# Kernel optimization log

Measured on AMD Instinct MI355X. Metric: run time of the kernel, lower is better.

The kernel has to match this reference:

```python
import jax, jax.numpy as jnp
import numpy as np

INPUT_DIM = 64
HIDDEN = 256
BATCH = 256
SEQ = 512
LN_EPS = 1e-5


def setup_inputs() -> dict:
    key = jax.random.key(0)
    ks = jax.random.split(key, 10)
    def lin(k, fan_in, fan_out):
        bound = 1.0 / np.sqrt(fan_in)
        kw, kb = jax.random.split(k)
        W = jax.random.uniform(kw, (fan_in, fan_out), jnp.float32, -bound, bound)
        b = jax.random.uniform(kb, (fan_out,), jnp.float32, -bound, bound)
        return W, b
    x = jax.random.normal(ks[0], (BATCH, SEQ, INPUT_DIM), jnp.float32)
    # layer 0: input_dim -> hidden
    Wz0, bz0 = lin(ks[1], INPUT_DIM + HIDDEN, 3 * HIDDEN)
    Wc0, bc0 = lin(ks[2], INPUT_DIM + HIDDEN, HIDDEN)
    # layer 1: hidden -> hidden
    Wz1, bz1 = lin(ks[3], HIDDEN + HIDDEN, 3 * HIDDEN)
    Wc1, bc1 = lin(ks[4], HIDDEN + HIDDEN, HIDDEN)
    ln_gamma = jnp.ones((HIDDEN,), jnp.float32)
    ln_beta = jnp.zeros((HIDDEN,), jnp.float32)
    return {"x": x, "Wz0": Wz0, "bz0": bz0, "Wc0": Wc0, "bc0": bc0,
            "Wz1": Wz1, "bz1": bz1, "Wc1": Wc1, "bc1": bc1,
            "ln_gamma": ln_gamma, "ln_beta": ln_beta}


def _gru_cell(h, x_t, Wz, bz, Wc, bc):
    # combined = [h, x]  (hidden first, as in the torch code)
    combined = jnp.concatenate([h, x_t], axis=-1)
    gates = combined @ Wz + bz  # (B, 3H); third chunk is unused (as in source)
    z = jax.nn.sigmoid(gates[:, :HIDDEN])
    r = jax.nn.sigmoid(gates[:, HIDDEN:2 * HIDDEN])
    reset_combined = jnp.concatenate([r * h, x_t], axis=-1)
    h_tilde = jnp.tanh(reset_combined @ Wc + bc)
    return (1.0 - z) * h + z * h_tilde


def reference(x, Wz0, bz0, Wc0, bc0, Wz1, bz1, Wc1, bc1, ln_gamma, ln_beta):
    # sanitize: NaN -> 0, Inf -> sign * 10
    x = jnp.where(jnp.isnan(x), 0.0, x)
    x = jnp.where(jnp.isinf(x), jnp.sign(x) * 10.0, x)

    B = x.shape[0]
    h0 = jnp.zeros((B, HIDDEN), x.dtype)
    h1 = jnp.zeros((B, HIDDEN), x.dtype)

    def step(carry, x_t):
        h0, h1 = carry
        h0 = _gru_cell(h0, x_t, Wz0, bz0, Wc0, bc0)
        h1 = _gru_cell(h1, h0, Wz1, bz1, Wc1, bc1)
        return (h0, h1), None

    xs = jnp.swapaxes(x, 0, 1)  # (seq, batch, input_dim)
    (h0, h1), _ = jax.lax.scan(step, (h0, h1), xs)

    # LayerNorm on final top-layer hidden state
    mean = jnp.mean(h1, axis=-1, keepdims=True)
    var = jnp.var(h1, axis=-1, keepdims=True)
    enc = (h1 - mean) * jax.lax.rsqrt(var + LN_EPS) * ln_gamma + ln_beta
    return enc
```

## Files before the change

kernel.cpp:

```cpp
#include <hip/hip_runtime.h>


#define SEQL 512
#define CH 8
#define NCH 64
#define DEPTH 4

#define RB0  1310720u
#define GSTR 1048576u
#define CTRB (RB0 + 16u * GSTR)

typedef __bf16 bf16x8 __attribute__((ext_vector_type(8)));
typedef float f32x4 __attribute__((ext_vector_type(4)));
typedef unsigned int u32x4 __attribute__((ext_vector_type(4)));
typedef unsigned long long u64;

__device__ __forceinline__ unsigned short f2bf(float f) {
  unsigned int u = __builtin_bit_cast(unsigned int, f);
  u += 0x7fffu + ((u >> 16) & 1u);
  return (unsigned short)(u >> 16);
}
__device__ __forceinline__ float bf2f(unsigned short u) {
  unsigned int v = ((unsigned int)u) << 16;
  return __builtin_bit_cast(float, v);
}
__device__ __forceinline__ float sigm(float x) { return 1.0f / (1.0f + __expf(-x)); }
__device__ __forceinline__ float tanh_(float x) { return 1.0f - 2.0f / (__expf(2.0f * x) + 1.0f); }
__device__ __forceinline__ float sanit(float v) {
  if (!(v == v)) return 0.f;
  if (isinf(v)) return v > 0.f ? 10.f : -10.f;
  return v;
}

__device__ __forceinline__ void st8(u64* p, u64 v) {
  __hip_atomic_store(p, v, __ATOMIC_RELAXED, __HIP_MEMORY_SCOPE_AGENT);
}

__device__ __forceinline__ void ld_frame8(const unsigned short* base, int lane, u32x4* c) {
  const char* p0 = (const char*)base + lane * 16;
  const char* p4 = p0 + 4096;
  asm volatile(
      "global_load_dwordx4 %0, %8, off sc0 sc1\n\t"
      "global_load_dwordx4 %1, %8, off offset:1024 sc0 sc1\n\t"
      "global_load_dwordx4 %2, %8, off offset:2048 sc0 sc1\n\t"
      "global_load_dwordx4 %3, %8, off offset:3072 sc0 sc1\n\t"
      "global_load_dwordx4 %4, %9, off sc0 sc1\n\t"
      "global_load_dwordx4 %5, %9, off offset:1024 sc0 sc1\n\t"
      "global_load_dwordx4 %6, %9, off offset:2048 sc0 sc1\n\t"
      "global_load_dwordx4 %7, %9, off offset:3072 sc0 sc1\n\t"
      "s_waitcnt vmcnt(0)"
      : "=&v"(c[0]), "=&v"(c[1]), "=&v"(c[2]), "=&v"(c[3]),
        "=&v"(c[4]), "=&v"(c[5]), "=&v"(c[6]), "=&v"(c[7])
      : "v"(p0), "v"(p4)
      : "memory");
}
__device__ __forceinline__ void ld_part12(const unsigned short* pf, int wave, int lane,
                                          u64* z, u64* r, u64* c) {
  const char* p0 = (const char*)pf + ((4 * wave) * 64 + lane) * 8;
  const char* p1 = p0 + 8192;
  const char* p2 = p0 + 16384;
  asm volatile(
      "global_load_dwordx2 %0, %12, off sc0 sc1\n\t"
      "global_load_dwordx2 %1, %12, off offset:512 sc0 sc1\n\t"
      "global_load_dwordx2 %2, %12, off offset:1024 sc0 sc1\n\t"
      "global_load_dwordx2 %3, %12, off offset:1536 sc0 sc1\n\t"
      "global_load_dwordx2 %4, %13, off sc0 sc1\n\t"
      "global_load_dwordx2 %5, %13, off offset:512 sc0 sc1\n\t"
      "global_load_dwordx2 %6, %13, off offset:1024 sc0 sc1\n\t"
      "global_load_dwordx2 %7, %13, off offset:1536 sc0 sc1\n\t"
      "global_load_dwordx2 %8, %14, off sc0 sc1\n\t"
      "global_load_dwordx2 %9, %14, off offset:512 sc0 sc1\n\t"
      "global_load_dwordx2 %10, %14, off offset:1024 sc0 sc1\n\t"
      "global_load_dwordx2 %11, %14, off offset:1536 sc0 sc1\n\t"
      "s_waitcnt vmcnt(0)"
      : "=&v"(z[0]), "=&v"(z[1]), "=&v"(z[2]), "=&v"(z[3]),
        "=&v"(r[0]), "=&v"(r[1]), "=&v"(r[2]), "=&v"(r[3]),
        "=&v"(c[0]), "=&v"(c[1]), "=&v"(c[2]), "=&v"(c[3])
      : "v"(p0), "v"(p1), "v"(p2)
      : "memory");
}

__global__ __launch_bounds__(256) void prep_weights(
    const float* __restrict__ Wz0, const float* __restrict__ Wc0,
    const float* __restrict__ Wz1, const float* __restrict__ Wc1,
    unsigned short* __restrict__ ws) {
  int idx = blockIdx.x * 256 + threadIdx.x;
  const float* W;
  int stride, KT, base;
  if (idx < 163840)      { W = Wz0; stride = 768; KT = 10; base = 0; }
  else if (idx < 245760) { W = Wc0; stride = 256; KT = 10; base = 163840; idx -= 163840; }
  else if (idx < 507904) { W = Wz1; stride = 768; KT = 16; base = 245760; idx -= 245760; }
  else                   { W = Wc1; stride = 256; KT = 16; base = 507904; idx -= 507904; }
  int tile = idx >> 9;
  int t = idx & 511;
  int nt = tile / KT;
  int kt = tile - nt * KT;
  int n15 = t & 15;
  int klocal = t >> 4;
  int k = (kt << 5) + klocal;
  int n = (nt << 4) + n15;
  int lane = ((klocal >> 3) << 4) | n15;
  int j = klocal & 7;
  ws[base + (tile << 9) + (lane << 3) + j] = f2bf(W[k * stride + n]);
}

__device__ __forceinline__ void waitge(int* p, int v, int tid) {
  __syncthreads();
  if (tid == 0) {
    long it = 0;
    while (__hip_atomic_load(p, __ATOMIC_RELAXED, __HIP_MEMORY_SCOPE_AGENT) < v) {
      __builtin_amdgcn_s_sleep(1);
      if (++it > (1L << 24)) break;
    }
  }
  __syncthreads();
}
__device__ __forceinline__ void publish(int* p, int v, int tid) {
  asm volatile("s_waitcnt vmcnt(0)" ::: "memory");
  __syncthreads();
  if (tid == 0) __hip_atomic_store(p, v, __ATOMIC_RELAXED, __HIP_MEMORY_SCOPE_AGENT);
}

#define DLOC(c) ((((c) >> 5) << 9) + (((((c) >> 3) & 3) << 4) + (quad << 2)) * 8 + ((c) & 7))
#define MFMA(a, b, c) __builtin_amdgcn_mfma_f32_16x16x32_bf16((a), (b), (c), 0, 0, 0)

union UB  { u32x4 q; bf16x8 v; };
union UB8 { u64 q; ushort4 s; };

__global__ __launch_bounds__(256, 1) void gru_pipe(
    const float* __restrict__ x,
    const float* __restrict__ bz0, const float* __restrict__ bc0,
    const float* __restrict__ bz1, const float* __restrict__ bc1,
    const float* __restrict__ gamma, const float* __restrict__ beta,
    const unsigned short* __restrict__ wsw,
    unsigned short* __restrict__ gws,
    float* __restrict__ out) {
  __shared__ __align__(16) unsigned short lds[75776];
  const int tid  = threadIdx.x;
  const int wave = tid >> 6;
  const int lane = tid & 63;
  const int l15  = lane & 15;
  const int quad = lane >> 4;
  const int stage = blockIdx.x >> 4;
  const int g     = blockIdx.x & 15;
  const int row0  = g << 4;

  const bf16x8* __restrict__ wsv = (const bf16x8*)wsw;
  unsigned short* ringh = gws + (RB0 >> 1) + (size_t)g * (GSTR >> 1);
  unsigned short* ringp = ringh + 131072;
  int* ctr = (int*)((char*)gws + CTRB) + g * 16;

  if (stage == 0) {
    unsigned short* h0f  = lds;
    unsigned short* rh0f = lds + 4096;
    unsigned short* xf   = lds + 8192;
    unsigned short* xw   = lds + 10240;
    unsigned short* cw0  = lds + 59392;
    for (int u = tid; u < 6144; u += 256) {
      int flat = u << 3, ti = flat >> 9, q = flat & 511, srct;
      if (ti < 64) srct = (ti >> 1) * 10 + 8 + (ti & 1);
      else         srct = 320 + ((ti - 64) >> 1) * 10 + 8 + (ti & 1);
      *(uint4*)(xw + flat) = *(const uint4*)(wsw + srct * 512 + q);
    }
    for (int u = tid; u < 2048; u += 256) {
      int flat = u << 3, ti = flat >> 9, q = flat & 511;
      int srct = 320 + (ti >> 1) * 10 + 6 + (ti & 1);
      *(uint4*)(cw0 + flat) = *(const uint4*)(wsw + srct * 512 + q);
    }
    for (int i = tid; i < 4096; i += 256) h0f[i] = 0;

    bf16x8 pz[4][8], pr[4][8], pc[4][6];
#pragma unroll
    for (int j = 0; j < 4; ++j) {
      const int zt = 4 * wave + j;
#pragma unroll
      for (int k = 0; k < 8; ++k) {
        pz[j][k] = wsv[(zt * 10 + k) * 64 + lane];
        pr[j][k] = wsv[((16 + zt) * 10 + k) * 64 + lane];
      }
#pragma unroll
      for (int k = 0; k < 6; ++k)
        pc[j][k] = wsv[(320 + zt * 10 + k) * 64 + lane];
    }
#pragma unroll
    for (int j = 0; j < 4; ++j) {
#pragma unroll
      for (int k = 0; k < 8; ++k)
        asm volatile("" : "+a"(pz[j][k]), "+a"(pr[j][k]));
#pragma unroll
      for (int k = 0; k < 6; ++k)
        asm volatile("" : "+v"(pc[j][k]));
    }

    float bzz[4], bzr[4], bcc[4];
    int dloc[4];
#pragma unroll
    for (int j = 0; j < 4; ++j) {
      const int col = 64 * wave + 16 * j + l15;
      bzz[j] = bz0[col]; bzr[j] = bz0[256 + col]; bcc[j] = bc0[col];
      dloc[j] = DLOC(col);
    }
    f32x4 h0s[4] = {{0,0,0,0},{0,0,0,0},{0,0,0,0},{0,0,0,0}};

    const int xrow = tid >> 4, c4 = (tid & 15) << 2;
    const float* xp = x + (size_t)(row0 + xrow) * (SEQL * 64) + c4;
    const int xbase = ((c4 >> 5) << 9) + ((((c4 >> 3) & 3) << 4) + xrow) * 8 + (c4 & 7);
    {
      float4 xv = *(const float4*)xp;
      xf[xbase] = f2bf(sanit(xv.x)); xf[xbase + 1] = f2bf(sanit(xv.y));
      xf[xbase + 2] = f2bf(sanit(xv.z)); xf[xbase + 3] = f2bf(sanit(xv.w));
    }
    __syncthreads();

    for (int ch = 0; ch < NCH; ++ch) {
      if (ch >= DEPTH) waitge(ctr + 2, ch - (DEPTH - 1), tid);
      unsigned short* slot = ringh + (ch & (DEPTH - 1)) * (CH * 4096);
      for (int s = 0; s < CH; ++s) {
        const int t = (ch << 3) + s;
        if (s > 0) {
          u64* dst = (u64*)(slot + (s - 1) * 4096);
          const u64* src = (const u64*)h0f;
#pragma unroll
          for (int q = 0; q < 4; ++q) st8(dst + tid + 256 * q, src[tid + 256 * q]);
        }
        const unsigned short* xb = xf + ((t & 1) << 10);
        const bool havex = (t + 1 < SEQL);
        float4 xn;
        if (havex) xn = *(const float4*)(xp + (t + 1) * 64);

        f32x4 za[4], ra[4];
#pragma unroll
        for (int j = 0; j < 4; ++j) { za[j] = {bzz[j],bzz[j],bzz[j],bzz[j]}; ra[j] = {bzr[j],bzr[j],bzr[j],bzr[j]}; }
#pragma unroll
        for (int k = 0; k < 8; ++k) {
          bf16x8 a = *(const bf16x8*)(h0f + (k << 9) + (lane << 3));
#pragma unroll
          for (int j = 0; j < 4; ++j) { za[j] = MFMA(a, pz[j][k], za[j]); ra[j] = MFMA(a, pr[j][k], ra[j]); }
        }
#pragma unroll
        for (int k = 0; k < 2; ++k) {
          bf16x8 a = *(const bf16x8*)(xb + (k << 9) + (lane << 3));
#pragma unroll
          for (int j = 0; j < 4; ++j) {
            bf16x8 bz_ = *(const bf16x8*)(xw + ((((4 * wave + j) << 1) | k) << 9) + (lane << 3));
            bf16x8 br_ = *(const bf16x8*)(xw + ((((16 + 4 * wave + j) << 1) | k) << 9) + (lane << 3));
            za[j] = MFMA(a, bz_, za[j]); ra[j] = MFMA(a, br_, ra[j]);
          }
        }
        float zg[4][4];
#pragma unroll
        for (int j = 0; j < 4; ++j)
#pragma unroll
          for (int i = 0; i < 4; ++i) {
            zg[j][i] = sigm(za[j][i]);
            rh0f[dloc[j] + i * 8] = f2bf(sigm(ra[j][i]) * h0s[j][i]);
          }
        __syncthreads();

        f32x4 ca[4];
#pragma unroll
        for (int j = 0; j < 4; ++j) ca[j] = {bcc[j],bcc[j],bcc[j],bcc[j]};
#pragma unroll
        for (int k = 0; k < 6; ++k) {
          bf16x8 a = *(const bf16x8*)(rh0f + (k << 9) + (lane << 3));
#pragma unroll
          for (int j = 0; j < 4; ++j) ca[j] = MFMA(a, pc[j][k], ca[j]);
        }
#pragma unroll
        for (int kk = 0; kk < 2; ++kk) {
          bf16x8 a = *(const bf16x8*)(rh0f + ((6 + kk) << 9) + (lane << 3));
#pragma unroll
          for (int j = 0; j < 4; ++j) {
            bf16x8 bc_ = *(const bf16x8*)(cw0 + ((((4 * wave + j) << 1) | kk) << 9) + (lane << 3));
            ca[j] = MFMA(a, bc_, ca[j]);
          }
        }
#pragma unroll
        for (int k = 0; k < 2; ++k) {
          bf16x8 a = *(const bf16x8*)(xb + (k << 9) + (lane << 3));
#pragma unroll
          for (int j = 0; j < 4; ++j) {
            bf16x8 bc_ = *(const bf16x8*)(xw + 32768 + ((((4 * wave + j) << 1) | k) << 9) + (lane << 3));
            ca[j] = MFMA(a, bc_, ca[j]);
          }
        }
#pragma unroll
        for (int j = 0; j < 4; ++j)
#pragma unroll
          for (int i = 0; i < 4; ++i) {
            float ht = tanh_(ca[j][i]);
            float hn = h0s[j][i] + zg[j][i] * (ht - h0s[j][i]);
            h0s[j][i] = hn;
            h0f[dloc[j] + i * 8] = f2bf(hn);
          }
        if (havex) {
          unsigned short* xb1 = xf + (((t + 1) & 1) << 10);
          xb1[xbase] = f2bf(sanit(xn.x)); xb1[xbase + 1] = f2bf(sanit(xn.y));
          xb1[xbase + 2] = f2bf(sanit(xn.z)); xb1[xbase + 3] = f2bf(sanit(xn.w));
        }
        __syncthreads();
      }
      {
        u64* dst = (u64*)(slot + 7 * 4096);
        const u64* src = (const u64*)h0f;
#pragma unroll
        for (int q = 0; q < 4; ++q) st8(dst + tid + 256 * q, src[tid + 256 * q]);
      }
      publish(ctr + 0, ch + 1, tid);
    }
  } else if (stage == 1) {
    unsigned short* cwB = lds;
    for (int u = tid; u < 2048; u += 256) {
      int flat = u << 3, ti = flat >> 9, q = flat & 511;
      int srct = 992 + (ti >> 1) * 16 + 14 + (ti & 1);
      *(uint4*)(cwB + flat) = *(const uint4*)(wsw + srct * 512 + q);
    }
    __syncthreads();

    bf16x8 p1[4][8], p2[4][8], p3[4][6];
#pragma unroll
    for (int j = 0; j < 4; ++j) {
      const int nt = 4 * wave + j;
#pragma unroll
      for (int k = 0; k < 8; ++k) {
        p1[j][k] = wsv[(480 + nt * 16 + 8 + k) * 64 + lane];
        p2[j][k] = wsv[(480 + (16 + nt) * 16 + 8 + k) * 64 + lane];
      }
#pragma unroll
      for (int k = 0; k < 6; ++k)
        p3[j][k] = wsv[(992 + nt * 16 + 8 + k) * 64 + lane];
    }
#pragma unroll
    for (int j = 0; j < 4; ++j) {
#pragma unroll
      for (int k = 0; k < 8; ++k)
        asm volatile("" : "+a"(p1[j][k]), "+a"(p2[j][k]));
#pragma unroll
      for (int k = 0; k < 6; ++k)
        asm volatile("" : "+v"(p3[j][k]));
    }
    float b1[4], b2[4], b3[4];
#pragma unroll
    for (int j = 0; j < 4; ++j) {
      const int col = 64 * wave + 16 * j + l15;
      b1[j] = bz1[col]; b2[j] = bz1[256 + col]; b3[j] = bc1[col];
    }
    for (int ch = 0; ch < NCH; ++ch) {
      waitge(ctr + 0, ch + 1, tid);
      if (ch >= DEPTH) waitge(ctr + 3, ch - (DEPTH - 1), tid);
      const unsigned short* hslot = ringh + (ch & (DEPTH - 1)) * (CH * 4096);
      unsigned short* pslot = ringp + (ch & (DEPTH - 1)) * (CH * 12288);
      for (int s = 0; s < CH; ++s) {
        u32x4 cf[8];
        ld_frame8(hslot + s * 4096, lane, cf);
        f32x4 za[4] = {{0,0,0,0},{0,0,0,0},{0,0,0,0},{0,0,0,0}};
        f32x4 ra[4] = {{0,0,0,0},{0,0,0,0},{0,0,0,0},{0,0,0,0}};
        f32x4 ca[4] = {{0,0,0,0},{0,0,0,0},{0,0,0,0},{0,0,0,0}};
#pragma unroll
        for (int k = 0; k < 8; ++k) {
          UB ub; ub.q = cf[k];
          bf16x8 a = ub.v;
#pragma unroll
          for (int j = 0; j < 4; ++j) {
            za[j] = MFMA(a, p1[j][k], za[j]);
            ra[j] = MFMA(a, p2[j][k], ra[j]);
            if (k < 6) ca[j] = MFMA(a, p3[j][k], ca[j]);
          }
        }
#pragma unroll
        for (int kk = 0; kk < 2; ++kk) {
          UB ub; ub.q = cf[6 + kk];
          bf16x8 a = ub.v;
#pragma unroll
          for (int j = 0; j < 4; ++j) {
            bf16x8 bc_ = *(const bf16x8*)(cwB + ((((4 * wave + j) << 1) | kk) << 9) + (lane << 3));
            ca[j] = MFMA(a, bc_, ca[j]);
          }
        }
        u64* pf = (u64*)(pslot + s * 12288);
#pragma unroll
        for (int j = 0; j < 4; ++j) {
          ushort4 vz, vr, vc;
          vz.x = f2bf(za[j][0] + b1[j]); vz.y = f2bf(za[j][1] + b1[j]);
          vz.z = f2bf(za[j][2] + b1[j]); vz.w = f2bf(za[j][3] + b1[j]);
          vr.x = f2bf(ra[j][0] + b2[j]); vr.y = f2bf(ra[j][1] + b2[j]);
          vr.z = f2bf(ra[j][2] + b2[j]); vr.w = f2bf(ra[j][3] + b2[j]);
          vc.x = f2bf(ca[j][0] + b3[j]); vc.y = f2bf(ca[j][1] + b3[j]);
          vc.z = f2bf(ca[j][2] + b3[j]); vc.w = f2bf(ca[j][3] + b3[j]);
          st8(pf + (4 * wave + j) * 64 + lane,      __builtin_bit_cast(u64, vz));
          st8(pf + (16 + 4 * wave + j) * 64 + lane, __builtin_bit_cast(u64, vr));
          st8(pf + (32 + 4 * wave + j) * 64 + lane, __builtin_bit_cast(u64, vc));
        }
      }
      publish(ctr + 1, ch + 1, tid);
      if (tid == 0)
        __hip_atomic_store(ctr + 2, ch + 1, __ATOMIC_RELAXED, __HIP_MEMORY_SCOPE_AGENT);
    }
  } else {
    unsigned short* h1f  = lds;
    unsigned short* rh1f = lds + 4096;
    unsigned short* cwC  = lds + 8192;
    for (int u = tid; u < 2048; u += 256) {
      int flat = u << 3, ti = flat >> 9, q = flat & 511;
      int srct = 992 + (ti >> 1) * 16 + 6 + (ti & 1);
      *(uint4*)(cwC + flat) = *(const uint4*)(wsw + srct * 512 + q);
    }
    bf16x8 q1[4][8], q2[4][8], q3[4][6];
#pragma unroll
    for (int j = 0; j < 4; ++j) {
      const int nt = 4 * wave + j;
#pragma unroll
      for (int k = 0; k < 8; ++k) {
        q1[j][k] = wsv[(480 + nt * 16 + k) * 64 + lane];
        q2[j][k] = wsv[(480 + (16 + nt) * 16 + k) * 64 + lane];
      }
#pragma unroll
      for (int k = 0; k < 6; ++k)
        q3[j][k] = wsv[(992 + nt * 16 + k) * 64 + lane];
    }
#pragma unroll
    for (int j = 0; j < 4; ++j) {
#pragma unroll
      for (int k = 0; k < 8; ++k)
        asm volatile("" : "+a"(q1[j][k]), "+a"(q2[j][k]));
#pragma unroll
      for (int k = 0; k < 6; ++k)
        asm volatile("" : "+v"(q3[j][k]));
    }
    for (int i = tid; i < 4096; i += 256) h1f[i] = 0;
    int dloc[4];
#pragma unroll
    for (int j = 0; j < 4; ++j) dloc[j] = DLOC(64 * wave + 16 * j + l15);
    f32x4 h1s[4] = {{0,0,0,0},{0,0,0,0},{0,0,0,0},{0,0,0,0}};
    __syncthreads();

    for (int ch = 0; ch < NCH; ++ch) {
      waitge(ctr + 1, ch + 1, tid);
      const unsigned short* pslot = ringp + (ch & (DEPTH - 1)) * (CH * 12288);
      for (int s = 0; s < CH; ++s) {
        u64 zq[4], rq[4], cq[4];
        ld_part12(pslot + s * 12288, wave, lane, zq, rq, cq);
        f32x4 za[4] = {{0,0,0,0},{0,0,0,0},{0,0,0,0},{0,0,0,0}};
        f32x4 ra[4] = {{0,0,0,0},{0,0,0,0},{0,0,0,0},{0,0,0,0}};
#pragma unroll
        for (int k = 0; k < 8; ++k) {
          bf16x8 a = *(const bf16x8*)(h1f + (k << 9) + (lane << 3));
#pragma unroll
          for (int j = 0; j < 4; ++j) { za[j] = MFMA(a, q1[j][k], za[j]); ra[j] = MFMA(a, q2[j][k], ra[j]); }
        }
        float zg[4][4];
#pragma unroll
        for (int j = 0; j < 4; ++j) {
          UB8 uz, ur; uz.q = zq[j]; ur.q = rq[j];
#pragma unroll
          for (int i = 0; i < 4; ++i) {
            zg[j][i] = sigm(za[j][i] + bf2f(((const unsigned short*)&uz.s)[i]));
            float r = sigm(ra[j][i] + bf2f(((const unsigned short*)&ur.s)[i]));
            rh1f[dloc[j] + i * 8] = f2bf(r * h1s[j][i]);
          }
        }
        __syncthreads();

        f32x4 ca[4] = {{0,0,0,0},{0,0,0,0},{0,0,0,0},{0,0,0,0}};
#pragma unroll
        for (int k = 0; k < 6; ++k) {
          bf16x8 a = *(const bf16x8*)(rh1f + (k << 9) + (lane << 3));
#pragma unroll
          for (int j = 0; j < 4; ++j) ca[j] = MFMA(a, q3[j][k], ca[j]);
        }
#pragma unroll
        for (int kk = 0; kk < 2; ++kk) {
          bf16x8 a = *(const bf16x8*)(rh1f + ((6 + kk) << 9) + (lane << 3));
#pragma unroll
          for (int j = 0; j < 4; ++j) {
            bf16x8 bc_ = *(const bf16x8*)(cwC + ((((4 * wave + j) << 1) | kk) << 9) + (lane << 3));
            ca[j] = MFMA(a, bc_, ca[j]);
          }
        }
#pragma unroll
        for (int j = 0; j < 4; ++j) {
          UB8 uc; uc.q = cq[j];
#pragma unroll
          for (int i = 0; i < 4; ++i) {
            float ht = tanh_(ca[j][i] + bf2f(((const unsigned short*)&uc.s)[i]));
            float hn = h1s[j][i] + zg[j][i] * (ht - h1s[j][i]);
            h1s[j][i] = hn;
            h1f[dloc[j] + i * 8] = f2bf(hn);
          }
        }
        __syncthreads();
      }
      publish(ctr + 3, ch + 1, tid);
    }

    float* h1buf = (float*)lds;
#pragma unroll
    for (int j = 0; j < 4; ++j)
#pragma unroll
      for (int i = 0; i < 4; ++i)
        h1buf[(quad * 4 + i) * 256 + 64 * wave + 16 * j + l15] = h1s[j][i];
    __syncthreads();

    const int r = tid >> 4, cl = tid & 15;
    float v[16], s = 0.f, sq = 0.f;
#pragma unroll
    for (int jj = 0; jj < 16; ++jj) {
      v[jj] = h1buf[r * 256 + cl + (jj << 4)];
      s += v[jj]; sq += v[jj] * v[jj];
    }
#pragma unroll
    for (int off = 8; off > 0; off >>= 1) {
      s  += __shfl_xor(s, off);
      sq += __shfl_xor(sq, off);
    }
    const float mean = s * (1.f / 256.f);
    const float var  = sq * (1.f / 256.f) - mean * mean;
    const float rstd = rsqrtf(var + 1e-5f);
    float* op = out + (size_t)(row0 + r) * 256;
#pragma unroll
    for (int jj = 0; jj < 16; ++jj) {
      const int c = cl + (jj << 4);
      op[c] = (v[jj] - mean) * rstd * gamma[c] + beta[c];
    }
  }
}

extern "C" void kernel_launch(void* const* d_in, const int* in_sizes, int n_in,
                              void* d_out, int out_size, void* d_ws, size_t ws_size,
                              hipStream_t stream) {
  const float* x     = (const float*)d_in[0];
  const float* Wz0   = (const float*)d_in[1];
  const float* bz0   = (const float*)d_in[2];
  const float* Wc0   = (const float*)d_in[3];
  const float* bc0   = (const float*)d_in[4];
  const float* Wz1   = (const float*)d_in[5];
  const float* bz1   = (const float*)d_in[6];
  const float* Wc1   = (const float*)d_in[7];
  const float* bc1   = (const float*)d_in[8];
  const float* gamma = (const float*)d_in[9];
  const float* beta  = (const float*)d_in[10];
  unsigned short* ws = (unsigned short*)d_ws;
  float* out = (float*)d_out;

  hipMemsetAsync((char*)d_ws + CTRB, 0, 1024, stream);
  hipLaunchKernelGGL(prep_weights, dim3(2496), dim3(256), 0, stream, Wz0, Wc0, Wz1, Wc1, ws);
  hipLaunchKernelGGL(gru_pipe, dim3(48), dim3(256), 0, stream,
                     x, bz0, bc0, bz1, bc1, gamma, beta, ws, ws, out);
}
```

Measured before the change: 2.629 ms.

## Double workgroup size to 8 waves, halving output column tiles per wave

Result: faster. 2.331 ms (-11.3%).

```diff
diff --git a/kernel.cpp b/kernel.cpp
--- a/kernel.cpp
+++ b/kernel.cpp
@@ -54,28 +54,21 @@
       : "v"(p0), "v"(p4)
       : "memory");
 }
-__device__ __forceinline__ void ld_part12(const unsigned short* pf, int wave, int lane,
-                                          u64* z, u64* r, u64* c) {
-  const char* p0 = (const char*)pf + ((4 * wave) * 64 + lane) * 8;
+__device__ __forceinline__ void ld_part6(const unsigned short* pf, int wave, int lane,
+                                         u64* z, u64* r, u64* c) {
+  const char* p0 = (const char*)pf + ((2 * wave) * 64 + lane) * 8;
   const char* p1 = p0 + 8192;
   const char* p2 = p0 + 16384;
   asm volatile(
-      "global_load_dwordx2 %0, %12, off sc0 sc1\n\t"
-      "global_load_dwordx2 %1, %12, off offset:512 sc0 sc1\n\t"
-      "global_load_dwordx2 %2, %12, off offset:1024 sc0 sc1\n\t"
-      "global_load_dwordx2 %3, %12, off offset:1536 sc0 sc1\n\t"
-      "global_load_dwordx2 %4, %13, off sc0 sc1\n\t"
-      "global_load_dwordx2 %5, %13, off offset:512 sc0 sc1\n\t"
-      "global_load_dwordx2 %6, %13, off offset:1024 sc0 sc1\n\t"
-      "global_load_dwordx2 %7, %13, off offset:1536 sc0 sc1\n\t"
-      "global_load_dwordx2 %8, %14, off sc0 sc1\n\t"
-      "global_load_dwordx2 %9, %14, off offset:512 sc0 sc1\n\t"
-      "global_load_dwordx2 %10, %14, off offset:1024 sc0 sc1\n\t"
-      "global_load_dwordx2 %11, %14, off offset:1536 sc0 sc1\n\t"
+      "global_load_dwordx2 %0, %6, off sc0 sc1\n\t"
+      "global_load_dwordx2 %1, %6, off offset:512 sc0 sc1\n\t"
+      "global_load_dwordx2 %2, %7, off sc0 sc1\n\t"
+      "global_load_dwordx2 %3, %7, off offset:512 sc0 sc1\n\t"
+      "global_load_dwordx2 %4, %8, off sc0 sc1\n\t"
+      "global_load_dwordx2 %5, %8, off offset:512 sc0 sc1\n\t"
       "s_waitcnt vmcnt(0)"
-      : "=&v"(z[0]), "=&v"(z[1]), "=&v"(z[2]), "=&v"(z[3]),
-        "=&v"(r[0]), "=&v"(r[1]), "=&v"(r[2]), "=&v"(r[3]),
-        "=&v"(c[0]), "=&v"(c[1]), "=&v"(c[2]), "=&v"(c[3])
+      : "=&v"(z[0]), "=&v"(z[1]), "=&v"(r[0]), "=&v"(r[1]),
+        "=&v"(c[0]), "=&v"(c[1])
       : "v"(p0), "v"(p1), "v"(p2)
       : "memory");
 }
@@ -127,7 +120,7 @@
 union UB  { u32x4 q; bf16x8 v; };
 union UB8 { u64 q; ushort4 s; };
 
-__global__ __launch_bounds__(256, 1) void gru_pipe(
+__global__ __launch_bounds__(512, 2) void gru_pipe(
     const float* __restrict__ x,
     const float* __restrict__ bz0, const float* __restrict__ bc0,
     const float* __restrict__ bz1, const float* __restrict__ bc1,
@@ -156,23 +149,23 @@
     unsigned short* xf   = lds + 8192;
     unsigned short* xw   = lds + 10240;
     unsigned short* cw0  = lds + 59392;
-    for (int u = tid; u < 6144; u += 256) {
+    for (int u = tid; u < 6144; u += 512) {
       int flat = u << 3, ti = flat >> 9, q = flat & 511, srct;
       if (ti < 64) srct = (ti >> 1) * 10 + 8 + (ti & 1);
       else         srct = 320 + ((ti - 64) >> 1) * 10 + 8 + (ti & 1);
       *(uint4*)(xw + flat) = *(const uint4*)(wsw + srct * 512 + q);
     }
-    for (int u = tid; u < 2048; u += 256) {
+    for (int u = tid; u < 2048; u += 512) {
       int flat = u << 3, ti = flat >> 9, q = flat & 511;
       int srct = 320 + (ti >> 1) * 10 + 6 + (ti & 1);
       *(uint4*)(cw0 + flat) = *(const uint4*)(wsw + srct * 512 + q);
     }
-    for (int i = tid; i < 4096; i += 256) h0f[i] = 0;
-
-    bf16x8 pz[4][8], pr[4][8], pc[4][6];
-#pragma unroll
-    for (int j = 0; j < 4; ++j) {
-      const int zt = 4 * wave + j;
+    for (int i = tid; i < 4096; i += 512) h0f[i] = 0;
+
+    bf16x8 pz[2][8], pr[2][8], pc[2][6];
+#pragma unroll
+    for (int j = 0; j < 2; ++j) {
+      const int zt = 2 * wave + j;
 #pragma unroll
       for (int k = 0; k < 8; ++k) {
         pz[j][k] = wsv[(zt * 10 + k) * 64 + lane];
@@ -183,29 +176,29 @@
         pc[j][k] = wsv[(320 + zt * 10 + k) * 64 + lane];
     }
 #pragma unroll
-    for (int j = 0; j < 4; ++j) {
+    for (int j = 0; j < 2; ++j) {
 #pragma unroll
       for (int k = 0; k < 8; ++k)
         asm volatile("" : "+a"(pz[j][k]), "+a"(pr[j][k]));
 #pragma unroll
       for (int k = 0; k < 6; ++k)
-        asm volatile("" : "+v"(pc[j][k]));
-    }
-
-    float bzz[4], bzr[4], bcc[4];
-    int dloc[4];
-#pragma unroll
-    for (int j = 0; j < 4; ++j) {
-      const int col = 64 * wave + 16 * j + l15;
+        asm volatile("" : "+a"(pc[j][k]));
+    }
+
+    float bzz[2], bzr[2], bcc[2];
+    int dloc[2];
+#pragma unroll
+    for (int j = 0; j < 2; ++j) {
+      const int col = 32 * wave + 16 * j + l15;
       bzz[j] = bz0[col]; bzr[j] = bz0[256 + col]; bcc[j] = bc0[col];
       dloc[j] = DLOC(col);
     }
-    f32x4 h0s[4] = {{0,0,0,0},{0,0,0,0},{0,0,0,0},{0,0,0,0}};
-
-    const int xrow = tid >> 4, c4 = (tid & 15) << 2;
+    f32x4 h0s[2] = {{0,0,0,0},{0,0,0,0}};
+
+    const int xrow = (tid >> 4) & 15, c4 = (tid & 15) << 2;
     const float* xp = x + (size_t)(row0 + xrow) * (SEQL * 64) + c4;
     const int xbase = ((c4 >> 5) << 9) + ((((c4 >> 3) & 3) << 4) + xrow) * 8 + (c4 & 7);
-    {
+    if (tid < 256) {
       float4 xv = *(const float4*)xp;
       xf[xbase] = f2bf(sanit(xv.x)); xf[xbase + 1] = f2bf(sanit(xv.y));
       xf[xbase + 2] = f2bf(sanit(xv.z)); xf[xbase + 3] = f2bf(sanit(xv.w));
@@ -221,35 +214,35 @@
           u64* dst = (u64*)(slot + (s - 1) * 4096);
           const u64* src = (const u64*)h0f;
 #pragma unroll
-          for (int q = 0; q < 4; ++q) st8(dst + tid + 256 * q, src[tid + 256 * q]);
+          for (int q = 0; q < 2; ++q) st8(dst + tid + 512 * q, src[tid + 512 * q]);
         }
         const unsigned short* xb = xf + ((t & 1) << 10);
-        const bool havex = (t + 1 < SEQL);
+        const bool havex = (t + 1 < SEQL) && (tid < 256);
         float4 xn;
         if (havex) xn = *(const float4*)(xp + (t + 1) * 64);
 
-        f32x4 za[4], ra[4];
-#pragma unroll
-        for (int j = 0; j < 4; ++j) { za[j] = {bzz[j],bzz[j],bzz[j],bzz[j]}; ra[j] = {bzr[j],bzr[j],bzr[j],bzr[j]}; }
+        f32x4 za[2], ra[2];
+#pragma unroll
+        for (int j = 0; j < 2; ++j) { za[j] = {bzz[j],bzz[j],bzz[j],bzz[j]}; ra[j] = {bzr[j],bzr[j],bzr[j],bzr[j]}; }
 #pragma unroll
         for (int k = 0; k < 8; ++k) {
           bf16x8 a = *(const bf16x8*)(h0f + (k << 9) + (lane << 3));
 #pragma unroll
-          for (int j = 0; j < 4; ++j) { za[j] = MFMA(a, pz[j][k], za[j]); ra[j] = MFMA(a, pr[j][k], ra[j]); }
+          for (int j = 0; j < 2; ++j) { za[j] = MFMA(a, pz[j][k], za[j]); ra[j] = MFMA(a, pr[j][k], ra[j]); }
         }
 #pragma unroll
         for (int k = 0; k < 2; ++k) {
           bf16x8 a = *(const bf16x8*)(xb + (k << 9) + (lane << 3));
 #pragma unroll
-          for (int j = 0; j < 4; ++j) {
-            bf16x8 bz_ = *(const bf16x8*)(xw + ((((4 * wave + j) << 1) | k) << 9) + (lane << 3));
-            bf16x8 br_ = *(const bf16x8*)(xw + ((((16 + 4 * wave + j) << 1) | k) << 9) + (lane << 3));
+          for (int j = 0; j < 2; ++j) {
+            bf16x8 bz_ = *(const bf16x8*)(xw + ((((2 * wave + j) << 1) | k) << 9) + (lane << 3));
+            bf16x8 br_ = *(const bf16x8*)(xw + ((((16 + 2 * wave + j) << 1) | k) << 9) + (lane << 3));
             za[j] = MFMA(a, bz_, za[j]); ra[j] = MFMA(a, br_, ra[j]);
           }
         }
-        float zg[4][4];
-#pragma unroll
-        for (int j = 0; j < 4; ++j)
+        float zg[2][4];
+#pragma unroll
+        for (int j = 0; j < 2; ++j)
 #pragma unroll
           for (int i = 0; i < 4; ++i) {
             zg[j][i] = sigm(za[j][i]);
@@ -257,21 +250,21 @@
           }
         __syncthreads();
 
-        f32x4 ca[4];
-#pragma unroll
-        for (int j = 0; j < 4; ++j) ca[j] = {bcc[j],bcc[j],bcc[j],bcc[j]};
+        f32x4 ca[2];
+#pragma unroll
+        for (int j = 0; j < 2; ++j) ca[j] = {bcc[j],bcc[j],bcc[j],bcc[j]};
 #pragma unroll
         for (int k = 0; k < 6; ++k) {
           bf16x8 a = *(const bf16x8*)(rh0f + (k << 9) + (lane << 3));
 #pragma unroll
-          for (int j = 0; j < 4; ++j) ca[j] = MFMA(a, pc[j][k], ca[j]);
+          for (int j = 0; j < 2; ++j) ca[j] = MFMA(a, pc[j][k], ca[j]);
         }
 #pragma unroll
         for (int kk = 0; kk < 2; ++kk) {
           bf16x8 a = *(const bf16x8*)(rh0f + ((6 + kk) << 9) + (lane << 3));
 #pragma unroll
-          for (int j = 0; j < 4; ++j) {
-            bf16x8 bc_ = *(const bf16x8*)(cw0 + ((((4 * wave + j) << 1) | kk) << 9) + (lane << 3));
+          for (int j = 0; j < 2; ++j) {
+            bf16x8 bc_ = *(const bf16x8*)(cw0 + ((((2 * wave + j) << 1) | kk) << 9) + (lane << 3));
             ca[j] = MFMA(a, bc_, ca[j]);
           }
         }
@@ -279,13 +272,13 @@
         for (int k = 0; k < 2; ++k) {
           bf16x8 a = *(const bf16x8*)(xb + (k << 9) + (lane << 3));
 #pragma unroll
-          for (int j = 0; j < 4; ++j) {
-            bf16x8 bc_ = *(const bf16x8*)(xw + 32768 + ((((4 * wave + j) << 1) | k) << 9) + (lane << 3));
+          for (int j = 0; j < 2; ++j) {
+            bf16x8 bc_ = *(const bf16x8*)(xw + 32768 + ((((2 * wave + j) << 1) | k) << 9) + (lane << 3));
             ca[j] = MFMA(a, bc_, ca[j]);
           }
         }
 #pragma unroll
-        for (int j = 0; j < 4; ++j)
+        for (int j = 0; j < 2; ++j)
 #pragma unroll
           for (int i = 0; i < 4; ++i) {
             float ht = tanh_(ca[j][i]);
@@ -304,23 +297,23 @@
         u64* dst = (u64*)(slot + 7 * 4096);
         const u64* src = (const u64*)h0f;
 #pragma unroll
-        for (int q = 0; q < 4; ++q) st8(dst + tid + 256 * q, src[tid + 256 * q]);
+        for (int q = 0; q < 2; ++q) st8(dst + tid + 512 * q, src[tid + 512 * q]);
       }
       publish(ctr + 0, ch + 1, tid);
     }
   } else if (stage == 1) {
     unsigned short* cwB = lds;
-    for (int u = tid; u < 2048; u += 256) {
+    for (int u = tid; u < 2048; u += 512) {
       int flat = u << 3, ti = flat >> 9, q = flat & 511;
       int srct = 992 + (ti >> 1) * 16 + 14 + (ti & 1);
       *(uint4*)(cwB + flat) = *(const uint4*)(wsw + srct * 512 + q);
     }
     __syncthreads();
 
-    bf16x8 p1[4][8], p2[4][8], p3[4][6];
-#pragma unroll
-    for (int j = 0; j < 4; ++j) {
-      const int nt = 4 * wave + j;
+    bf16x8 p1[2][8], p2[2][8], p3[2][6];
+#pragma unroll
+    for (int j = 0; j < 2; ++j) {
+      const int nt = 2 * wave + j;
 #pragma unroll
       for (int k = 0; k < 8; ++k) {
         p1[j][k] = wsv[(480 + nt * 16 + 8 + k) * 64 + lane];
@@ -331,18 +324,18 @@
         p3[j][k] = wsv[(992 + nt * 16 + 8 + k) * 64 + lane];
     }
 #pragma unroll
-    for (int j = 0; j < 4; ++j) {
+    for (int j = 0; j < 2; ++j) {
 #pragma unroll
       for (int k = 0; k < 8; ++k)
         asm volatile("" : "+a"(p1[j][k]), "+a"(p2[j][k]));
 #pragma unroll
       for (int k = 0; k < 6; ++k)
-        asm volatile("" : "+v"(p3[j][k]));
-    }
-    float b1[4], b2[4], b3[4];
-#pragma unroll
-    for (int j = 0; j < 4; ++j) {
-      const int col = 64 * wave + 16 * j + l15;
+        asm volatile("" : "+a"(p3[j][k]));
+    }
+    float b1[2], b2[2], b3[2];
+#pragma unroll
+    for (int j = 0; j < 2; ++j) {
+      const int col = 32 * wave + 16 * j + l15;
       b1[j] = bz1[col]; b2[j] = bz1[256 + col]; b3[j] = bc1[col];
     }
     for (int ch = 0; ch < NCH; ++ch) {
@@ -353,15 +346,15 @@
       for (int s = 0; s < CH; ++s) {
         u32x4 cf[8];
         ld_frame8(hslot + s * 4096, lane, cf);
-        f32x4 za[4] = {{0,0,0,0},{0,0,0,0},{0,0,0,0},{0,0,0,0}};
-        f32x4 ra[4] = {{0,0,0,0},{0,0,0,0},{0,0,0,0},{0,0,0,0}};
-        f32x4 ca[4] = {{0,0,0,0},{0,0,0,0},{0,0,0,0},{0,0,0,0}};
+        f32x4 za[2] = {{0,0,0,0},{0,0,0,0}};
+        f32x4 ra[2] = {{0,0,0,0},{0,0,0,0}};
+        f32x4 ca[2] = {{0,0,0,0},{0,0,0,0}};
 #pragma unroll
         for (int k = 0; k < 8; ++k) {
           UB ub; ub.q = cf[k];
           bf16x8 a = ub.v;
 #pragma unroll
-          for (int j = 0; j < 4; ++j) {
+          for (int j = 0; j < 2; ++j) {
             za[j] = MFMA(a, p1[j][k], za[j]);
             ra[j] = MFMA(a, p2[j][k], ra[j]);
             if (k < 6) ca[j] = MFMA(a, p3[j][k], ca[j]);
@@ -372,14 +365,14 @@
           UB ub; ub.q = cf[6 + kk];
           bf16x8 a = ub.v;
 #pragma unroll
-          for (int j = 0; j < 4; ++j) {
-            bf16x8 bc_ = *(const bf16x8*)(cwB + ((((4 * wave + j) << 1) | kk) << 9) + (lane << 3));
+          for (int j = 0; j < 2; ++j) {
+            bf16x8 bc_ = *(const bf16x8*)(cwB + ((((2 * wave + j) << 1) | kk) << 9) + (lane << 3));
             ca[j] = MFMA(a, bc_, ca[j]);
           }
         }
         u64* pf = (u64*)(pslot + s * 12288);
 #pragma unroll
-        for (int j = 0; j < 4; ++j) {
+        for (int j = 0; j < 2; ++j) {
           ushort4 vz, vr, vc;
           vz.x = f2bf(za[j][0] + b1[j]); vz.y = f2bf(za[j][1] + b1[j]);
           vz.z = f2bf(za[j][2] + b1[j]); vz.w = f2bf(za[j][3] + b1[j]);
@@ -387,9 +380,9 @@
           vr.z = f2bf(ra[j][2] + b2[j]); vr.w = f2bf(ra[j][3] + b2[j]);
           vc.x = f2bf(ca[j][0] + b3[j]); vc.y = f2bf(ca[j][1] + b3[j]);
           vc.z = f2bf(ca[j][2] + b3[j]); vc.w = f2bf(ca[j][3] + b3[j]);
-          st8(pf + (4 * wave + j) * 64 + lane,      __builtin_bit_cast(u64, vz));
-          st8(pf + (16 + 4 * wave + j) * 64 + lane, __builtin_bit_cast(u64, vr));
-          st8(pf + (32 + 4 * wave + j) * 64 + lane, __builtin_bit_cast(u64, vc));
+          st8(pf + (2 * wave + j) * 64 + lane,      __builtin_bit_cast(u64, vz));
+          st8(pf + (16 + 2 * wave + j) * 64 + lane, __builtin_bit_cast(u64, vr));
+          st8(pf + (32 + 2 * wave + j) * 64 + lane, __builtin_bit_cast(u64, vc));
         }
       }
       publish(ctr + 1, ch + 1, tid);
@@ -400,15 +393,15 @@
     unsigned short* h1f  = lds;
     unsigned short* rh1f = lds + 4096;
     unsigned short* cwC  = lds + 8192;
-    for (int u = tid; u < 2048; u += 256) {
+    for (int u = tid; u < 2048; u += 512) {
       int flat = u << 3, ti = flat >> 9, q = flat & 511;
       int srct = 992 + (ti >> 1) * 16 + 6 + (ti & 1);
       *(uint4*)(cwC + flat) = *(const uint4*)(wsw + srct * 512 + q);
     }
-    bf16x8 q1[4][8], q2[4][8], q3[4][6];
-#pragma unroll
-    for (int j = 0; j < 4; ++j) {
-      const int nt = 4 * wave + j;
+    bf16x8 q1[2][8], q2[2][8], q3[2][6];
+#pragma unroll
+    for (int j = 0; j < 2; ++j) {
+      const int nt = 2 * wave + j;
 #pragma unroll
       for (int k = 0; k < 8; ++k) {
         q1[j][k] = wsv[(480 + nt * 16 + k) * 64 + lane];
@@ -419,38 +412,38 @@
         q3[j][k] = wsv[(992 + nt * 16 + k) * 64 + lane];
     }
 #pragma unroll
-    for (int j = 0; j < 4; ++j) {
+    for (int j = 0; j < 2; ++j) {
 #pragma unroll
       for (int k = 0; k < 8; ++k)
         asm volatile("" : "+a"(q1[j][k]), "+a"(q2[j][k]));
 #pragma unroll
       for (int k = 0; k < 6; ++k)
-        asm volatile("" : "+v"(q3[j][k]));
-    }
-    for (int i = tid; i < 4096; i += 256) h1f[i] = 0;
-    int dloc[4];
-#pragma unroll
-    for (int j = 0; j < 4; ++j) dloc[j] = DLOC(64 * wave + 16 * j + l15);
-    f32x4 h1s[4] = {{0,0,0,0},{0,0,0,0},{0,0,0,0},{0,0,0,0}};
+        asm volatile("" : "+a"(q3[j][k]));
+    }
+    for (int i = tid; i < 4096; i += 512) h1f[i] = 0;
+    int dloc[2];
+#pragma unroll
+    for (int j = 0; j < 2; ++j) dloc[j] = DLOC(32 * wave + 16 * j + l15);
+    f32x4 h1s[2] = {{0,0,0,0},{0,0,0,0}};
     __syncthreads();
 
     for (int ch = 0; ch < NCH; ++ch) {
       waitge(ctr + 1, ch + 1, tid);
       const unsigned short* pslot = ringp + (ch & (DEPTH - 1)) * (CH * 12288);
       for (int s = 0; s < CH; ++s) {
-        u64 zq[4], rq[4], cq[4];
-        ld_part12(pslot + s * 12288, wave, lane, zq, rq, cq);
-        f32x4 za[4] = {{0,0,0,0},{0,0,0,0},{0,0,0,0},{0,0,0,0}};
-        f32x4 ra[4] = {{0,0,0,0},{0,0,0,0},{0,0,0,0},{0,0,0,0}};
+        u64 zq[2], rq[2], cq[2];
+        ld_part6(pslot + s * 12288, wave, lane, zq, rq, cq);
+        f32x4 za[2] = {{0,0,0,0},{0,0,0,0}};
+        f32x4 ra[2] = {{0,0,0,0},{0,0,0,0}};
 #pragma unroll
         for (int k = 0; k < 8; ++k) {
           bf16x8 a = *(const bf16x8*)(h1f + (k << 9) + (lane << 3));
 #pragma unroll
-          for (int j = 0; j < 4; ++j) { za[j] = MFMA(a, q1[j][k], za[j]); ra[j] = MFMA(a, q2[j][k], ra[j]); }
-        }
-        float zg[4][4];
-#pragma unroll
-        for (int j = 0; j < 4; ++j) {
+          for (int j = 0; j < 2; ++j) { za[j] = MFMA(a, q1[j][k], za[j]); ra[j] = MFMA(a, q2[j][k], ra[j]); }
+        }
+        float zg[2][4];
+#pragma unroll
+        for (int j = 0; j < 2; ++j) {
           UB8 uz, ur; uz.q = zq[j]; ur.q = rq[j];
 #pragma unroll
           for (int i = 0; i < 4; ++i) {
@@ -461,24 +454,24 @@
         }
         __syncthreads();
 
-        f32x4 ca[4] = {{0,0,0,0},{0,0,0,0},{0,0,0,0},{0,0,0,0}};
+        f32x4 ca[2] = {{0,0,0,0},{0,0,0,0}};
 #pragma unroll
         for (int k = 0; k < 6; ++k) {
           bf16x8 a = *(const bf16x8*)(rh1f + (k << 9) + (lane << 3));
 #pragma unroll
-          for (int j = 0; j < 4; ++j) ca[j] = MFMA(a, q3[j][k], ca[j]);
+          for (int j = 0; j < 2; ++j) ca[j] = MFMA(a, q3[j][k], ca[j]);
         }
 #pragma unroll
         for (int kk = 0; kk < 2; ++kk) {
           bf16x8 a = *(const bf16x8*)(rh1f + ((6 + kk) << 9) + (lane << 3));
 #pragma unroll
-          for (int j = 0; j < 4; ++j) {
-            bf16x8 bc_ = *(const bf16x8*)(cwC + ((((4 * wave + j) << 1) | kk) << 9) + (lane << 3));
+          for (int j = 0; j < 2; ++j) {
+            bf16x8 bc_ = *(const bf16x8*)(cwC + ((((2 * wave + j) << 1) | kk) << 9) + (lane << 3));
             ca[j] = MFMA(a, bc_, ca[j]);
           }
         }
 #pragma unroll
-        for (int j = 0; j < 4; ++j) {
+        for (int j = 0; j < 2; ++j) {
           UB8 uc; uc.q = cq[j];
 #pragma unroll
           for (int i = 0; i < 4; ++i) {
@@ -495,32 +488,34 @@
 
     float* h1buf = (float*)lds;
 #pragma unroll
-    for (int j = 0; j < 4; ++j)
+    for (int j = 0; j < 2; ++j)
 #pragma unroll
       for (int i = 0; i < 4; ++i)
-        h1buf[(quad * 4 + i) * 256 + 64 * wave + 16 * j + l15] = h1s[j][i];
+        h1buf[(quad * 4 + i) * 256 + 32 * wave + 16 * j + l15] = h1s[j][i];
     __syncthreads();
 
-    const int r = tid >> 4, cl = tid & 15;
-    float v[16], s = 0.f, sq = 0.f;
-#pragma unroll
-    for (int jj = 0; jj < 16; ++jj) {
-      v[jj] = h1buf[r * 256 + cl + (jj << 4)];
-      s += v[jj]; sq += v[jj] * v[jj];
-    }
-#pragma unroll
-    for (int off = 8; off > 0; off >>= 1) {
-      s  += __shfl_xor(s, off);
-      sq += __shfl_xor(sq, off);
-    }
-    const float mean = s * (1.f / 256.f);
-    const float var  = sq * (1.f / 256.f) - mean * mean;
-    const float rstd = rsqrtf(var + 1e-5f);
-    float* op = out + (size_t)(row0 + r) * 256;
-#pragma unroll
-    for (int jj = 0; jj < 16; ++jj) {
-      const int c = cl + (jj << 4);
-      op[c] = (v[jj] - mean) * rstd * gamma[c] + beta[c];
+    if (tid < 256) {
+      const int r = tid >> 4, cl = tid & 15;
+      float v[16], s = 0.f, sq = 0.f;
+#pragma unroll
+      for (int jj = 0; jj < 16; ++jj) {
+        v[jj] = h1buf[r * 256 + cl + (jj << 4)];
+        s += v[jj]; sq += v[jj] * v[jj];
+      }
+#pragma unroll
+      for (int off = 8; off > 0; off >>= 1) {
+        s  += __shfl_xor(s, off);
+        sq += __shfl_xor(sq, off);
+      }
+      const float mean = s * (1.f / 256.f);
+      const float var  = sq * (1.f / 256.f) - mean * mean;
+      const float rstd = rsqrtf(var + 1e-5f);
+      float* op = out + (size_t)(row0 + r) * 256;
+#pragma unroll
+      for (int jj = 0; jj < 16; ++jj) {
+        const int c = cl + (jj << 4);
+        op[c] = (v[jj] - mean) * rstd * gamma[c] + beta[c];
+      }
     }
   }
 }
@@ -544,6 +539,6 @@
 
   hipMemsetAsync((char*)d_ws + CTRB, 0, 1024, stream);
   hipLaunchKernelGGL(prep_weights, dim3(2496), dim3(256), 0, stream, Wz0, Wc0, Wz1, Wc1, ws);
-  hipLaunchKernelGGL(gru_pipe, dim3(48), dim3(256), 0, stream,
+  hipLaunchKernelGGL(gru_pipe, dim3(48), dim3(512), 0, stream,
                      x, bz0, bc0, bz1, bc1, gamma, beta, ws, ws, out);
 }
```
